# Kernel optimization log

Hardware: AMD Instinct MI355X
Metric: run time of the kernel (lower is better)

The kernel has to match this reference:

```python
import jax, jax.numpy as jnp
import numpy as np

DIM = 256
HEADS = 8
HEAD_DIM = DIM // HEADS


def setup_inputs() -> dict:
    key = jax.random.key(0)
    ks = jax.random.split(key, 10)
    B, Nq, Nk, C = 2, 2048, 2048, DIM
    inp = {
        "query": jax.random.normal(ks[0], (B, Nq, C), jnp.float32),
        "key": jax.random.normal(ks[1], (B, Nk, C), jnp.float32),
        "value": jax.random.normal(ks[2], (B, Nk, C), jnp.float32),
        "qpos": jnp.zeros((B, Nq), jnp.int32),
        "kpos": jnp.zeros((B, Nk), jnp.int32),
        "mask": jax.random.randint(ks[3], (Nq, Nk), 0, 2) > 0,
        "similarities": jax.random.normal(ks[4], (B, HEADS, Nq, Nk), jnp.float32),
        # learned params (torch Linear stored here as [C_in, C_out]; no qkv bias)
        "Wq": jax.random.normal(ks[5], (C, C), jnp.float32) / np.sqrt(C),
        "Wk": jax.random.normal(ks[6], (C, C), jnp.float32) / np.sqrt(C),
        "Wv": jax.random.normal(ks[7], (C, C), jnp.float32) / np.sqrt(C),
        "Wp": jax.random.normal(ks[8], (C, C), jnp.float32) / np.sqrt(C),
        "bp": jax.random.normal(ks[9], (C,), jnp.float32) * 0.01,
    }
    return inp


def reference(query, key, value, qpos, kpos, mask, similarities, Wq, Wk, Wv, Wp, bp):
    B, Nq, C = query.shape
    Nk = key.shape[1]
    H, hd = HEADS, HEAD_DIM
    scale = hd ** -0.5
    # projections -> [B, N, H, hd] (rope is None, so qpos/kpos are unused)
    q = (query @ Wq).reshape(B, Nq, H, hd)
    k = (key @ Wk).reshape(B, Nk, H, hd)
    v = (value @ Wv).reshape(B, Nk, H, hd)
    # scores [B, H, Nq, Nk]
    attn = jnp.einsum("bqhd,bkhd->bhqk", q, k) * scale
    # mean-centered similarity bias (mean over heads, dim=1)
    attn = attn + (similarities - similarities.mean(axis=1, keepdims=True))
    # boolean mask: fill False positions with -inf, then softmax over keys
    attn = jnp.where(mask[None, None, :, :], attn, -jnp.inf)
    attn = jax.nn.softmax(attn, axis=-1)
    # AV -> [B, Nq, C], output projection
    x = jnp.einsum("bhqk,bkhd->bqhd", attn, v).reshape(B, Nq, C)
    return x @ Wp + bp
```

## Files before the change

kernel.cpp:

```cpp
#include <hip/hip_runtime.h>

#define B_  2
#define NQ  2048
#define NK  2048
#define C_  256
#define H_  8
#define HD  32
#define SPLIT 4
#define KSEG (NK / SPLIT)
#define KT   (KSEG / 32)
#define QT_  (NQ / 16)
#define PART_STRIDE 544

typedef float f32x4 __attribute__((ext_vector_type(4)));
typedef __bf16 bf16x8 __attribute__((ext_vector_type(8)));
typedef unsigned short ushort8 __attribute__((ext_vector_type(8)));

static __device__ __forceinline__ unsigned short f2bf(float f) {
    unsigned int u = __builtin_bit_cast(unsigned int, f);
    u += 0x7FFFu + ((u >> 16) & 1u);
    return (unsigned short)(u >> 16);
}
static __device__ __forceinline__ float bf2f(unsigned short h) {
    unsigned int u = ((unsigned int)h) << 16;
    return __builtin_bit_cast(float, u);
}
static __device__ __forceinline__ unsigned int split1(float f) {
    unsigned short h = f2bf(f);
    unsigned short l = f2bf(f - bf2f(h));
    return (unsigned int)h | ((unsigned int)l << 16);
}
static __device__ __forceinline__ bf16x8 ld_bf16x8(const unsigned short* p) {
    return __builtin_bit_cast(bf16x8, *(const ushort8*)p);
}

static __device__ __forceinline__ void barrier_lds() {
    __builtin_amdgcn_sched_barrier(0);
    asm volatile("s_waitcnt lgkmcnt(0)" ::: "memory");
    __builtin_amdgcn_s_barrier();
    __builtin_amdgcn_sched_barrier(0);
}

__global__ __launch_bounds__(256) void maskpack_kernel(const int* __restrict__ mask,
                                                       unsigned short* __restrict__ mb)
{
    const int qt = blockIdx.x;
    const int k  = blockIdx.y * 256 + threadIdx.x;
    unsigned int m = 0;
    #pragma unroll
    for (int r = 0; r < 16; ++r)
        m |= (mask[(size_t)(qt * 16 + r) * NK + k] ? 1u : 0u) << r;
    mb[(size_t)qt * NK + k] = (unsigned short)m;
}

__global__ __launch_bounds__(256) void proj_kernel(
        const float* __restrict__ query, const float* __restrict__ key,
        const float* __restrict__ value,
        const float* __restrict__ Wq, const float* __restrict__ Wk,
        const float* __restrict__ Wv,
        unsigned short* __restrict__ qbh, unsigned short* __restrict__ qbl,
        unsigned short* __restrict__ kbh, unsigned short* __restrict__ kbl,
        unsigned short* __restrict__ vbh, unsigned short* __restrict__ vbl)
{
    __shared__ unsigned short WtH[64][40];
    __shared__ unsigned short WtL[64][40];
    __shared__ unsigned short TrH[64][80];
    __shared__ unsigned short TrL[64][80];

    const int z = blockIdx.z;
    const float* X = (z == 0) ? query : (z == 1) ? key : value;
    const float* W = (z == 0) ? Wq    : (z == 1) ? Wk  : Wv;
    unsigned short* dh = (z == 0) ? qbh : (z == 1) ? kbh : vbh;
    unsigned short* dl = (z == 0) ? qbl : (z == 1) ? kbl : vbl;
    const int vmode = (z == 2);

    const int tid  = threadIdx.x;
    const int wave = tid >> 6;
    const int lane = tid & 63;
    const int n15  = lane & 15;
    const int quad = lane >> 4;
    const int m0   = blockIdx.x * 64;
    const int j0   = blockIdx.y * 64;

    f32x4 acc[4];
    acc[0] = 0.f; acc[1] = 0.f; acc[2] = 0.f; acc[3] = 0.f;

    const int sj  = tid >> 2;
    const int skc = (tid & 3) * 8;
    const float* __restrict__ xrow = X + (size_t)(m0 + wave * 16 + n15) * C_;

    for (int k0 = 0; k0 < C_; k0 += 32) {
        ushort8 wh, wl;
        #pragma unroll
        for (int i = 0; i < 8; ++i) {
            unsigned int p = split1(W[(size_t)(k0 + skc + i) * C_ + j0 + sj]);
            wh[i] = (unsigned short)p;
            wl[i] = (unsigned short)(p >> 16);
        }
        *(ushort8*)&WtH[sj][skc] = wh;
        *(ushort8*)&WtL[sj][skc] = wl;
        __syncthreads();

        f32x4 a0 = *(const f32x4*)(xrow + k0 + quad * 8);
        f32x4 a1 = *(const f32x4*)(xrow + k0 + quad * 8 + 4);
        ushort8 ah, al;
        #pragma unroll
        for (int i = 0; i < 4; ++i) {
            unsigned int p0 = split1(a0[i]);
            unsigned int p1 = split1(a1[i]);
            ah[i]     = (unsigned short)p0;  al[i]     = (unsigned short)(p0 >> 16);
            ah[i + 4] = (unsigned short)p1;  al[i + 4] = (unsigned short)(p1 >> 16);
        }
        bf16x8 Ah = __builtin_bit_cast(bf16x8, ah);
        bf16x8 Al = __builtin_bit_cast(bf16x8, al);

        #pragma unroll
        for (int f = 0; f < 4; ++f) {
            bf16x8 Bh = ld_bf16x8(&WtH[f * 16 + n15][quad * 8]);
            bf16x8 Bl = ld_bf16x8(&WtL[f * 16 + n15][quad * 8]);
            acc[f] = __builtin_amdgcn_mfma_f32_16x16x32_bf16(Al, Bl, acc[f], 0, 0, 0);
            acc[f] = __builtin_amdgcn_mfma_f32_16x16x32_bf16(Al, Bh, acc[f], 0, 0, 0);
            acc[f] = __builtin_amdgcn_mfma_f32_16x16x32_bf16(Ah, Bl, acc[f], 0, 0, 0);
            acc[f] = __builtin_amdgcn_mfma_f32_16x16x32_bf16(Ah, Bh, acc[f], 0, 0, 0);
        }
        __syncthreads();
    }

    if (vmode) {
        #pragma unroll
        for (int f = 0; f < 4; ++f) {
            const int jl = f * 16 + n15;
            #pragma unroll
            for (int r = 0; r < 4; ++r) {
                const int rowl = wave * 16 + quad * 4 + r;
                unsigned int p = split1(acc[f][r]);
                TrH[jl][rowl] = (unsigned short)p;
                TrL[jl][rowl] = (unsigned short)(p >> 16);
            }
        }
        __syncthreads();
        const int jl = tid >> 2, chunk = (tid & 3) * 16;
        const int j  = j0 + jl, h = j >> 5, dd = j & 31;
        const int bb = m0 >> 11;
        const size_t obase = (size_t)((bb * H_ + h) * HD + dd) * NK
                           + (m0 & 2047) + chunk;
        *(ushort8*)(dh + obase)     = *(const ushort8*)&TrH[jl][chunk];
        *(ushort8*)(dh + obase + 8) = *(const ushort8*)&TrH[jl][chunk + 8];
        *(ushort8*)(dl + obase)     = *(const ushort8*)&TrL[jl][chunk];
        *(ushort8*)(dl + obase + 8) = *(const ushort8*)&TrL[jl][chunk + 8];
    } else {
        #pragma unroll
        for (int f = 0; f < 4; ++f) {
            const int j = j0 + f * 16 + n15;
            const int h = j >> 5, dd = j & 31;
            #pragma unroll
            for (int r = 0; r < 4; ++r) {
                const int grow = m0 + wave * 16 + quad * 4 + r;
                const int b = grow >> 11, row = grow & 2047;
                unsigned int p = split1(acc[f][r]);
                size_t idx = (size_t)((b * H_ + h) * NK + row) * HD + dd;
                dh[idx] = (unsigned short)p;
                dl[idx] = (unsigned short)(p >> 16);
            }
        }
    }
}

__global__ __launch_bounds__(256) void outproj_kernel(const unsigned short* __restrict__ Xh,
                                                      const unsigned short* __restrict__ Xl,
                                                      const float* __restrict__ W,
                                                      const float* __restrict__ bias,
                                                      float* __restrict__ out)
{
    __shared__ unsigned short WtH[64][40];
    __shared__ unsigned short WtL[64][40];

    const int tid  = threadIdx.x;
    const int wave = tid >> 6;
    const int lane = tid & 63;
    const int n15  = lane & 15;
    const int quad = lane >> 4;
    const int m0   = blockIdx.x * 64;
    const int j0   = blockIdx.y * 64;

    f32x4 acc[4];
    acc[0] = 0.f; acc[1] = 0.f; acc[2] = 0.f; acc[3] = 0.f;

    const int sj  = tid >> 2;
    const int skc = (tid & 3) * 8;
    const size_t xoff = (size_t)(m0 + wave * 16 + n15) * C_;

    for (int k0 = 0; k0 < C_; k0 += 32) {
        ushort8 wh, wl;
        #pragma unroll
        for (int i = 0; i < 8; ++i) {
            unsigned int p = split1(W[(size_t)(k0 + skc + i) * C_ + j0 + sj]);
            wh[i] = (unsigned short)p;
            wl[i] = (unsigned short)(p >> 16);
        }
        *(ushort8*)&WtH[sj][skc] = wh;
        *(ushort8*)&WtL[sj][skc] = wl;
        __syncthreads();

        bf16x8 Ah = ld_bf16x8(Xh + xoff + k0 + quad * 8);
        bf16x8 Al = ld_bf16x8(Xl + xoff + k0 + quad * 8);

        #pragma unroll
        for (int f = 0; f < 4; ++f) {
            bf16x8 Bh = ld_bf16x8(&WtH[f * 16 + n15][quad * 8]);
            bf16x8 Bl = ld_bf16x8(&WtL[f * 16 + n15][quad * 8]);
            acc[f] = __builtin_amdgcn_mfma_f32_16x16x32_bf16(Al, Bl, acc[f], 0, 0, 0);
            acc[f] = __builtin_amdgcn_mfma_f32_16x16x32_bf16(Al, Bh, acc[f], 0, 0, 0);
            acc[f] = __builtin_amdgcn_mfma_f32_16x16x32_bf16(Ah, Bl, acc[f], 0, 0, 0);
            acc[f] = __builtin_amdgcn_mfma_f32_16x16x32_bf16(Ah, Bh, acc[f], 0, 0, 0);
        }
        __syncthreads();
    }

    #pragma unroll
    for (int f = 0; f < 4; ++f) {
        const int j = j0 + f * 16 + n15;
        const float bj = bias[j];
        #pragma unroll
        for (int r = 0; r < 4; ++r) {
            const int grow = m0 + wave * 16 + quad * 4 + r;
            out[(size_t)grow * C_ + j] = acc[f][r] + bj;
        }
    }
}

__global__ __launch_bounds__(512, 6) void attn_kernel(
        const unsigned short* __restrict__ qh, const unsigned short* __restrict__ ql,
        const unsigned short* __restrict__ kh, const unsigned short* __restrict__ kl,
        const unsigned short* __restrict__ vh, const unsigned short* __restrict__ vl,
        const float* __restrict__ sim, const unsigned short* __restrict__ maskb,
        float* __restrict__ part)
{
    __shared__ __align__(16) float simLds[2][H_][16][33];
    __shared__ float biasLds[16][33];
    __shared__ __align__(16) unsigned short pLds[H_][16 * 40];
    __shared__ unsigned short maskLds[KSEG];

    const int tid  = threadIdx.x;
    const int wave = tid >> 6;
    const int lane = tid & 63;
    const int n15  = lane & 15;
    const int quad = lane >> 4;

    const int wg   = blockIdx.x;
    const int s    = wg >> 8;
    const int rem  = wg & 255;
    const int b    = rem >> 7;
    const int qt   = rem & 127;
    const int q0   = qt * 16;
    const int kbeg = s * KSEG;

    const size_t bh   = (size_t)(b * H_ + wave);
    const size_t qoff = (bh * NQ + q0 + n15) * HD + quad * 8;
    const unsigned short* khb = kh + bh * NK * HD;
    const unsigned short* klb = kl + bh * NK * HD;
    const unsigned short* vhb = vh + bh * HD * NK;
    const unsigned short* vlb = vl + bh * HD * NK;
    const unsigned short* mkb = maskb + (size_t)qt * NK + kbeg;

    const int swr = lane >> 2, swc = (lane & 3) * 8;
    const float* gsim = sim + (bh * NQ + q0 + swr) * (size_t)NK + kbeg + swc;
    const int kk = tid & 31;

    const bf16x8 Qh = ld_bf16x8(qh + qoff);
    const bf16x8 Ql = ld_bf16x8(ql + qoff);

    f32x4 O0 = 0.f, O1 = 0.f;
    float m_r[4] = {0.f, 0.f, 0.f, 0.f};
    float l_r[4] = {0.f, 0.f, 0.f, 0.f};

    const float scale = 0.17677669529663687f;

    maskLds[tid] = mkb[tid];
    {
        f32x4 pA = *(const f32x4*)gsim;
        f32x4 pB = *(const f32x4*)(gsim + 4);
        float* sw0 = &simLds[0][wave][swr][swc];
        *(f32x4*)sw0       = pA;
        *(f32x4*)(sw0 + 4) = pB;
    }

    auto tile_body = [&](int it, bool pf) {
        const int cur = it & 1;
        const int k0  = kbeg + it * 32;

        barrier_lds();

        {
            const int qq = tid >> 5;
            float sum = 0.f;
            #pragma unroll
            for (int h = 0; h < H_; ++h) sum += simLds[cur][h][qq][kk];
            const unsigned short mw = maskLds[it * 32 + kk];
            biasLds[qq][kk] = ((mw >> qq) & 1) ? (-0.125f * sum) : -1e30f;
        }
        barrier_lds();

        const size_t koA = (size_t)(k0 + n15) * HD + quad * 8;
        const size_t koB = (size_t)(k0 + 16 + n15) * HD + quad * 8;
        bf16x8 Kh0 = ld_bf16x8(khb + koA), Kl0 = ld_bf16x8(klb + koA);
        bf16x8 Kh1 = ld_bf16x8(khb + koB), Kl1 = ld_bf16x8(klb + koB);
        __builtin_amdgcn_sched_barrier(0);
        f32x4 nA, nB;
        if (pf) {
            nA = *(const f32x4*)(gsim + (it + 1) * 32);
            nB = *(const f32x4*)(gsim + (it + 1) * 32 + 4);
        }
        __builtin_amdgcn_sched_barrier(0);

        f32x4 S0 = 0.f, S1 = 0.f;
        S0 = __builtin_amdgcn_mfma_f32_16x16x32_bf16(Ql, Kl0, S0, 0, 0, 0);
        S0 = __builtin_amdgcn_mfma_f32_16x16x32_bf16(Ql, Kh0, S0, 0, 0, 0);
        S0 = __builtin_amdgcn_mfma_f32_16x16x32_bf16(Qh, Kl0, S0, 0, 0, 0);
        S0 = __builtin_amdgcn_mfma_f32_16x16x32_bf16(Qh, Kh0, S0, 0, 0, 0);
        S1 = __builtin_amdgcn_mfma_f32_16x16x32_bf16(Ql, Kl1, S1, 0, 0, 0);
        S1 = __builtin_amdgcn_mfma_f32_16x16x32_bf16(Ql, Kh1, S1, 0, 0, 0);
        S1 = __builtin_amdgcn_mfma_f32_16x16x32_bf16(Qh, Kl1, S1, 0, 0, 0);
        S1 = __builtin_amdgcn_mfma_f32_16x16x32_bf16(Qh, Kh1, S1, 0, 0, 0);

        unsigned int u0[4], u1[4];
        #pragma unroll
        for (int r = 0; r < 4; ++r) {
            const int qq = quad * 4 + r;
            float s0 = S0[r] * scale + simLds[cur][wave][qq][n15]      + biasLds[qq][n15];
            float s1 = S1[r] * scale + simLds[cur][wave][qq][16 + n15] + biasLds[qq][16 + n15];

            float mx = fmaxf(s0, s1);
            #pragma unroll
            for (int off = 1; off < 16; off <<= 1) mx = fmaxf(mx, __shfl_xor(mx, off));
            const float mnew = fmaxf(m_r[r], mx);
            const float a  = __expf(m_r[r] - mnew);
            const float p0 = __expf(s0 - mnew);
            const float p1 = __expf(s1 - mnew);
            float sm = p0 + p1;
            #pragma unroll
            for (int off = 1; off < 16; off <<= 1) sm += __shfl_xor(sm, off);
            l_r[r] = l_r[r] * a + sm;
            m_r[r] = mnew;
            O0[r] *= a; O1[r] *= a;
            u0[r] = split1(p0); u1[r] = split1(p1);
        }

        __builtin_amdgcn_sched_barrier(0);
        const size_t voA = (size_t)n15 * NK + k0 + quad * 8;
        const size_t voB = (size_t)(16 + n15) * NK + k0 + quad * 8;
        bf16x8 Vh0 = ld_bf16x8(vhb + voA), Vl0 = ld_bf16x8(vlb + voA);
        bf16x8 Vh1 = ld_bf16x8(vhb + voB), Vl1 = ld_bf16x8(vlb + voB);
        __builtin_amdgcn_sched_barrier(0);

        unsigned short* pw = pLds[wave];
        #pragma unroll
        for (int r = 0; r < 4; ++r) {
            const int qq = quad * 4 + r;
            pw[qq * 40 + n15]      = (unsigned short)u0[r];
            pw[qq * 40 + 16 + n15] = (unsigned short)u1[r];
        }
        bf16x8 Ph = ld_bf16x8(pw + n15 * 40 + quad * 8);
        #pragma unroll
        for (int r = 0; r < 4; ++r) {
            const int qq = quad * 4 + r;
            pw[qq * 40 + n15]      = (unsigned short)(u0[r] >> 16);
            pw[qq * 40 + 16 + n15] = (unsigned short)(u1[r] >> 16);
        }
        bf16x8 Pl = ld_bf16x8(pw + n15 * 40 + quad * 8);

        O0 = __builtin_amdgcn_mfma_f32_16x16x32_bf16(Pl, Vl0, O0, 0, 0, 0);
        O0 = __builtin_amdgcn_mfma_f32_16x16x32_bf16(Pl, Vh0, O0, 0, 0, 0);
        O0 = __builtin_amdgcn_mfma_f32_16x16x32_bf16(Ph, Vl0, O0, 0, 0, 0);
        O0 = __builtin_amdgcn_mfma_f32_16x16x32_bf16(Ph, Vh0, O0, 0, 0, 0);
        O1 = __builtin_amdgcn_mfma_f32_16x16x32_bf16(Pl, Vl1, O1, 0, 0, 0);
        O1 = __builtin_amdgcn_mfma_f32_16x16x32_bf16(Pl, Vh1, O1, 0, 0, 0);
        O1 = __builtin_amdgcn_mfma_f32_16x16x32_bf16(Ph, Vl1, O1, 0, 0, 0);
        O1 = __builtin_amdgcn_mfma_f32_16x16x32_bf16(Ph, Vh1, O1, 0, 0, 0);

        if (pf) {
            float* swn = &simLds[cur ^ 1][wave][swr][swc];
            *(f32x4*)swn       = nA;
            *(f32x4*)(swn + 4) = nB;
        }
    };

    for (int it = 0; it < KT - 1; ++it) tile_body(it, true);
    tile_body(KT - 1, false);

    float* pb = part + (size_t)(((s * B_ + b) * H_ + wave) * QT_ + qt) * PART_STRIDE;
    #pragma unroll
    for (int r = 0; r < 4; ++r) {
        const int q = quad * 4 + r;
        pb[q * 32 + n15]      = O0[r];
        pb[q * 32 + 16 + n15] = O1[r];
        if (n15 == 0) {
            pb[512 + q] = m_r[r];
            pb[528 + q] = l_r[r];
        }
    }
}

__global__ __launch_bounds__(256) void combine_kernel(const float* __restrict__ part,
                                                      unsigned short* __restrict__ xh,
                                                      unsigned short* __restrict__ xl)
{
    const int wid  = blockIdx.x * 4 + (threadIdx.x >> 6);
    const int lane = threadIdx.x & 63;
    const int b  = wid >> 10;
    const int h  = (wid >> 7) & 7;
    const int qt = wid & 127;
    const int q  = lane >> 2;
    const int d0 = (lane & 3) * 8;

    float ms[SPLIT], ls[SPLIT];
    float mstar = -1e30f;
    #pragma unroll
    for (int s = 0; s < SPLIT; ++s) {
        const float* pb = part + (size_t)(((s * B_ + b) * H_ + h) * QT_ + qt) * PART_STRIDE;
        ms[s] = pb[512 + q];
        ls[s] = pb[528 + q];
        mstar = fmaxf(mstar, ms[s]);
    }
    f32x4 acc0 = 0.f, acc1 = 0.f;
    float lsum = 0.f;
    #pragma unroll
    for (int s = 0; s < SPLIT; ++s) {
        const float* pb = part + (size_t)(((s * B_ + b) * H_ + h) * QT_ + qt) * PART_STRIDE;
        const float w = __expf(ms[s] - mstar);
        lsum += w * ls[s];
        f32x4 o0 = *(const f32x4*)(pb + q * 32 + d0);
        f32x4 o1 = *(const f32x4*)(pb + q * 32 + d0 + 4);
        acc0 += w * o0;
        acc1 += w * o1;
    }
    const float inv = 1.0f / lsum;
    const size_t base = (size_t)(b * NQ + qt * 16 + q) * C_ + h * HD + d0;
    #pragma unroll
    for (int i = 0; i < 4; ++i) {
        unsigned int p0 = split1(acc0[i] * inv);
        unsigned int p1 = split1(acc1[i] * inv);
        xh[base + i]     = (unsigned short)p0;
        xl[base + i]     = (unsigned short)(p0 >> 16);
        xh[base + 4 + i] = (unsigned short)p1;
        xl[base + 4 + i] = (unsigned short)(p1 >> 16);
    }
}

extern "C" void kernel_launch(void* const* d_in, const int* in_sizes, int n_in,
                              void* d_out, int out_size, void* d_ws, size_t ws_size,
                              hipStream_t stream) {
    const float* query = (const float*)d_in[0];
    const float* key   = (const float*)d_in[1];
    const float* value = (const float*)d_in[2];
    const int*   mask  = (const int*)d_in[5];
    const float* sim   = (const float*)d_in[6];
    const float* Wq  = (const float*)d_in[7];
    const float* Wk  = (const float*)d_in[8];
    const float* Wv  = (const float*)d_in[9];
    const float* Wp  = (const float*)d_in[10];
    const float* bp  = (const float*)d_in[11];
    float* out = (float*)d_out;

    const size_t NEL = (size_t)B_ * H_ * NQ * HD;
    unsigned short* qbh = (unsigned short*)d_ws;
    unsigned short* qbl = qbh + NEL;
    unsigned short* kbh = qbl + NEL;
    unsigned short* kbl = kbh + NEL;
    unsigned short* vbh = kbl + NEL;
    unsigned short* vbl = vbh + NEL;
    unsigned short* xbh = vbl + NEL;
    unsigned short* xbl = xbh + NEL;
    float* part = (float*)(xbl + NEL);
    unsigned short* maskbW = (unsigned short*)(part
                            + (size_t)SPLIT * B_ * H_ * QT_ * PART_STRIDE);

    maskpack_kernel<<<dim3(QT_, NK / 256), 256, 0, stream>>>(mask, maskbW);
    proj_kernel<<<dim3(64, 4, 3), 256, 0, stream>>>(query, key, value, Wq, Wk, Wv,
                                                    qbh, qbl, kbh, kbl, vbh, vbl);
    attn_kernel<<<SPLIT * 256, 512, 0, stream>>>(qbh, qbl, kbh, kbl, vbh, vbl,
                                                 sim, maskbW, part);
    combine_kernel<<<512, 256, 0, stream>>>(part, xbh, xbl);
    outproj_kernel<<<dim3(64, 4), 256, 0, stream>>>(xbh, xbl, Wp, bp, out);
}
```

Before: 606.5 us.

## Use three uneven key splits and prefetch similarity tiles two steps ahead

```diff
diff --git a/kernel.cpp b/kernel.cpp
--- a/kernel.cpp
+++ b/kernel.cpp
@@ -6,9 +6,7 @@
 #define C_  256
 #define H_  8
 #define HD  32
-#define SPLIT 4
-#define KSEG (NK / SPLIT)
-#define KT   (KSEG / 32)
+#define SPLIT 3
 #define QT_  (NQ / 16)
 #define PART_STRIDE 544
 
@@ -239,7 +237,7 @@
     __shared__ __align__(16) float simLds[2][H_][16][33];
     __shared__ float biasLds[16][33];
     __shared__ __align__(16) unsigned short pLds[H_][16 * 40];
-    __shared__ unsigned short maskLds[KSEG];
+    __shared__ unsigned short maskLds[NK];
 
     const int tid  = threadIdx.x;
     const int wave = tid >> 6;
@@ -253,7 +251,8 @@
     const int b    = rem >> 7;
     const int qt   = rem & 127;
     const int q0   = qt * 16;
-    const int kbeg = s * KSEG;
+    const int tile_lo = (s == 0) ? 0  : (s == 1) ? 22 : 43;
+    const int nt      = (s == 0) ? 22 : 21;
 
     const size_t bh   = (size_t)(b * H_ + wave);
     const size_t qoff = (bh * NQ + q0 + n15) * HD + quad * 8;
@@ -261,10 +260,11 @@
     const unsigned short* klb = kl + bh * NK * HD;
     const unsigned short* vhb = vh + bh * HD * NK;
     const unsigned short* vlb = vl + bh * HD * NK;
-    const unsigned short* mkb = maskb + (size_t)qt * NK + kbeg;
+    const unsigned short* mrow = maskb + (size_t)qt * NK;
 
     const int swr = lane >> 2, swc = (lane & 3) * 8;
-    const float* gsim = sim + (bh * NQ + q0 + swr) * (size_t)NK + kbeg + swc;
+    const float* gsim = sim + (bh * NQ + q0 + swr) * (size_t)NK
+                            + tile_lo * 32 + swc;
     const int kk = tid & 31;
 
     const bf16x8 Qh = ld_bf16x8(qh + qoff);
@@ -276,7 +276,8 @@
 
     const float scale = 0.17677669529663687f;
 
-    maskLds[tid] = mkb[tid];
+    #pragma unroll
+    for (int i = 0; i < 4; ++i) maskLds[tid + i * 512] = mrow[tid + i * 512];
     {
         f32x4 pA = *(const f32x4*)gsim;
         f32x4 pB = *(const f32x4*)(gsim + 4);
@@ -284,10 +285,12 @@
         *(f32x4*)sw0       = pA;
         *(f32x4*)(sw0 + 4) = pB;
     }
-
-    auto tile_body = [&](int it, bool pf) {
+    f32x4 rA = *(const f32x4*)(gsim + 32);
+    f32x4 rB = *(const f32x4*)(gsim + 36);
+
+    auto tile_body = [&](int it, bool pf1, bool pf2) {
         const int cur = it & 1;
-        const int k0  = kbeg + it * 32;
+        const int k0  = (tile_lo + it) * 32;
 
         barrier_lds();
 
@@ -296,7 +299,7 @@
             float sum = 0.f;
             #pragma unroll
             for (int h = 0; h < H_; ++h) sum += simLds[cur][h][qq][kk];
-            const unsigned short mw = maskLds[it * 32 + kk];
+            const unsigned short mw = maskLds[k0 + kk];
             biasLds[qq][kk] = ((mw >> qq) & 1) ? (-0.125f * sum) : -1e30f;
         }
         barrier_lds();
@@ -305,12 +308,6 @@
         const size_t koB = (size_t)(k0 + 16 + n15) * HD + quad * 8;
         bf16x8 Kh0 = ld_bf16x8(khb + koA), Kl0 = ld_bf16x8(klb + koA);
         bf16x8 Kh1 = ld_bf16x8(khb + koB), Kl1 = ld_bf16x8(klb + koB);
-        __builtin_amdgcn_sched_barrier(0);
-        f32x4 nA, nB;
-        if (pf) {
-            nA = *(const f32x4*)(gsim + (it + 1) * 32);
-            nB = *(const f32x4*)(gsim + (it + 1) * 32 + 4);
-        }
         __builtin_amdgcn_sched_barrier(0);
 
         f32x4 S0 = 0.f, S1 = 0.f;
@@ -352,6 +349,12 @@
         bf16x8 Vh0 = ld_bf16x8(vhb + voA), Vl0 = ld_bf16x8(vlb + voA);
         bf16x8 Vh1 = ld_bf16x8(vhb + voB), Vl1 = ld_bf16x8(vlb + voB);
         __builtin_amdgcn_sched_barrier(0);
+        f32x4 nA, nB;
+        if (pf2) {
+            nA = *(const f32x4*)(gsim + (it + 2) * 32);
+            nB = *(const f32x4*)(gsim + (it + 2) * 32 + 4);
+        }
+        __builtin_amdgcn_sched_barrier(0);
 
         unsigned short* pw = pLds[wave];
         #pragma unroll
@@ -378,15 +381,17 @@
         O1 = __builtin_amdgcn_mfma_f32_16x16x32_bf16(Ph, Vl1, O1, 0, 0, 0);
         O1 = __builtin_amdgcn_mfma_f32_16x16x32_bf16(Ph, Vh1, O1, 0, 0, 0);
 
-        if (pf) {
+        if (pf1) {
             float* swn = &simLds[cur ^ 1][wave][swr][swc];
-            *(f32x4*)swn       = nA;
-            *(f32x4*)(swn + 4) = nB;
-        }
+            *(f32x4*)swn       = rA;
+            *(f32x4*)(swn + 4) = rB;
+        }
+        if (pf2) { rA = nA; rB = nB; }
     };
 
-    for (int it = 0; it < KT - 1; ++it) tile_body(it, true);
-    tile_body(KT - 1, false);
+    for (int it = 0; it < nt - 2; ++it) tile_body(it, true, true);
+    tile_body(nt - 2, true, false);
+    tile_body(nt - 1, false, false);
 
     float* pb = part + (size_t)(((s * B_ + b) * H_ + wave) * QT_ + qt) * PART_STRIDE;
     #pragma unroll
```

Result: slower. 743.1 us (+22.5%).
